# Kernel optimization log

Hardware: AMD Instinct MI355X
Metric: run time of the kernel (lower is better)

The kernel has to match this reference:

```python
import jax, jax.numpy as jnp
import numpy as np

G = 128        # grid resolution per axis (points are voxel centers on this grid)
N = 262144     # number of input points == number of output points
CIN = 16
COUT = 32


def _build_neighbors(inp_coords, out_coords):
    """Emulates FixedRadiusSearch(Linf, r=1.53*voxel) + invert_neighbors_list on a
    unit grid: for each output point and each of the 27 kernel taps t, find the
    (unique) input point at out_coord - (t-1), or -1 if that voxel is empty."""
    enc = lambda c: (c[:, 0].astype(np.int64) * G + c[:, 1]) * G + c[:, 2]
    inp_keys = enc(inp_coords)
    order = np.argsort(inp_keys)
    skeys = inp_keys[order]
    nbr = np.full((out_coords.shape[0], 27), -1, dtype=np.int32)
    k = 0
    for t0 in range(3):
        for t1 in range(3):
            for t2 in range(3):
                d = np.array([t0 - 1, t1 - 1, t2 - 1], dtype=np.int64)
                nc = out_coords - d  # input voxel s.t. (out - inp) == d
                valid = np.all((nc >= 0) & (nc < G), axis=1)
                keys = enc(np.clip(nc, 0, G - 1))
                pos = np.searchsorted(skeys, keys).clip(0, len(skeys) - 1)
                found = valid & (skeys[pos] == keys)
                nbr[:, k] = np.where(found, order[pos].astype(np.int32), -1)
                k += 1
    return nbr


def setup_inputs() -> dict:
    rng = np.random.default_rng(0)
    # unique voxels -> at most one point per voxel (regular-grid assumption)
    inp_keys = rng.choice(G ** 3, size=N, replace=False)
    out_keys = rng.choice(G ** 3, size=N, replace=False)
    dec = lambda kk: np.stack([kk // (G * G), (kk // G) % G, kk % G], axis=1).astype(np.int64)
    nbr_idx = jnp.asarray(_build_neighbors(dec(inp_keys), dec(out_keys)))

    key = jax.random.key(0)
    k1, k2 = jax.random.split(key)
    inp_features = jax.random.normal(k1, (N, CIN), dtype=jnp.float32)
    # matches kernel_initializer = uniform_(-0.05, 0.05)
    kernel = jax.random.uniform(k2, (3, 3, 3, CIN, COUT), dtype=jnp.float32,
                                minval=-0.05, maxval=0.05)
    bias = jnp.zeros((COUT,), dtype=jnp.float32)  # bias_initializer = zeros_
    return {"inp_features": inp_features, "kernel": kernel, "bias": bias,
            "nbr_idx": nbr_idx}


def reference(inp_features, kernel, bias, nbr_idx):
    # continuous_conv_transpose with interpolation='nearest_neighbor',
    # coordinate_mapping='identity', normalize=False on a unit grid:
    # out[j] = sum_t W[t] @ f[nbr(j, t)]  (missing taps contribute zero), + bias
    valid = (nbr_idx >= 0)
    idx = jnp.where(valid, nbr_idx, 0)
    gathered = inp_features[idx] * valid[..., None].astype(inp_features.dtype)  # [N,27,Cin]
    W = kernel.reshape(27, kernel.shape[-2], kernel.shape[-1])                  # [27,Cin,Cout]
    return jnp.einsum('nkc,kco->no', gathered, W) + bias
```

## Files before the change

### kernel.cpp

```cpp
#include <hip/hip_runtime.h>
#include <hip/hip_bf16.h>

#define NPTS  262144
#define CIN   16
#define COUT  32
#define NTAPS 27
#define BLK   512
#define DEPTH 12

typedef __attribute__((ext_vector_type(8)))  short short8v;
typedef __attribute__((ext_vector_type(16))) float f32x16;

__global__ __launch_bounds__(256) void cvt_feat_kernel(
    const float* __restrict__ feat, __hip_bfloat16* __restrict__ fb)
{
    const int i = blockIdx.x * 256 + threadIdx.x;
    const float4 x = ((const float4*)feat)[i];
    __hip_bfloat162* o = (__hip_bfloat162*)fb;
    o[2 * i]     = __float22bfloat162_rn(float2{x.x, x.y});
    o[2 * i + 1] = __float22bfloat162_rn(float2{x.z, x.w});
}

template<bool USE_WS>
__global__ __launch_bounds__(BLK, 3) void sct_mfma_kernel(
    const float* __restrict__ feat,
    const __hip_bfloat16* __restrict__ featb,
    const float* __restrict__ Wg,
    const float* __restrict__ bias,
    const int*   __restrict__ nbr,
    float*       __restrict__ out)
{
    __shared__ short bpack[NTAPS * 512];

    const int tid = threadIdx.x;
    for (int i = tid; i < NTAPS * 512; i += BLK) {
        const int tap  = i >> 9;
        const int r    = i & 511;
        const int ln   = r >> 3;
        const int e    = r & 7;
        const int cin  = ((ln >> 5) << 3) + e;
        const int cout = ln & 31;
        const __hip_bfloat16 h = __float2bfloat16(Wg[(tap * CIN + cin) * COUT + cout]);
        bpack[i] = *(const short*)&h;
    }
    __syncthreads();

    const int lane = tid & 63;
    const int wv   = tid >> 6;
    const int p0   = blockIdx.x * 256 + wv * 32;
    const int prow = lane & 31;
    const int g    = lane >> 5;
    const int* nb  = nbr + (long)(p0 + prow) * NTAPS;

    int nid[NTAPS];
    #pragma unroll
    for (int q = 0; q < 6; ++q) {
        const int4 v = *(const int4*)(nb + 4 * q);
        nid[4*q+0] = v.x; nid[4*q+1] = v.y; nid[4*q+2] = v.z; nid[4*q+3] = v.w;
    }
    {
        const int2 v2 = *(const int2*)(nb + 24);
        nid[24] = v2.x; nid[25] = v2.y; nid[26] = nb[26];
    }

    f32x16 acc;
    {
        const float b = bias[prow];
        #pragma unroll
        for (int r2 = 0; r2 < 16; ++r2) acc[r2] = b;
    }

    short8v af[DEPTH];

    auto gather1 = [&](int t, short8v& dst) {
        const int id = nid[t];
        short8v a = {};
        if (id >= 0) {
            if (USE_WS) {
                a = *(const short8v*)(featb + (long)id * CIN + g * 8);
            } else {
                const float4* fp = (const float4*)(feat + (long)id * CIN + g * 8);
                const float4 x = fp[0];
                const float4 y = fp[1];
                union { short8v v; __hip_bfloat162 h[4]; } u;
                u.h[0] = __float22bfloat162_rn(float2{x.x, x.y});
                u.h[1] = __float22bfloat162_rn(float2{x.z, x.w});
                u.h[2] = __float22bfloat162_rn(float2{y.x, y.y});
                u.h[3] = __float22bfloat162_rn(float2{y.z, y.w});
                a = u.v;
            }
        }
        dst = a;
    };

    #pragma unroll
    for (int t = 0; t < DEPTH; ++t) gather1(t, af[t]);

    #pragma unroll
    for (int t = 0; t < NTAPS; ++t) {
        const short8v bf = *(const short8v*)&bpack[(t << 9) + (lane << 3)];
        acc = __builtin_amdgcn_mfma_f32_32x32x16_bf16(af[t % DEPTH], bf, acc, 0, 0, 0);
        if (t + DEPTH < NTAPS) gather1(t + DEPTH, af[(t + DEPTH) % DEPTH]);
    }

    #pragma unroll
    for (int r2 = 0; r2 < 16; ++r2) {
        const int row = (r2 & 3) + 8 * (r2 >> 2) + 4 * g;
        out[(long)(p0 + row) * COUT + prow] = acc[r2];
    }
}

extern "C" void kernel_launch(void* const* d_in, const int* in_sizes, int n_in,
                              void* d_out, int out_size, void* d_ws, size_t ws_size,
                              hipStream_t stream) {
    const float* feat = (const float*)d_in[0];
    const float* Wg   = (const float*)d_in[1];
    const float* bias = (const float*)d_in[2];
    const int*   nbr  = (const int*)d_in[3];
    float*       out  = (float*)d_out;

    const size_t need = (size_t)NPTS * CIN * sizeof(__hip_bfloat16);
    if (ws_size >= need) {
        __hip_bfloat16* fb = (__hip_bfloat16*)d_ws;
        cvt_feat_kernel<<<NPTS * CIN / 4 / 256, 256, 0, stream>>>(feat, fb);
        sct_mfma_kernel<true><<<NPTS / 256, BLK, 0, stream>>>(feat, fb, Wg, bias, nbr, out);
    } else {
        sct_mfma_kernel<false><<<NPTS / 256, BLK, 0, stream>>>(feat, nullptr, Wg, bias, nbr, out);
    }
}
```

Baseline: 43.86 us.

## Precompute packed bf16 weight image in prep kernel and shrink blocks

The weight conversion and MFMA-layout packing moves out of every block into a one-off prep block, which writes a padded bf16 image to the workspace. Each conv block now fills LDS with a few vectorized 16-byte copies instead of strided scalar fp32 reads and converts. Blocks drop from 512 to 256 threads with a launch bound of 5, and gather depth falls from 12 to 8 to reduce register pressure. This is meant to raise occupancy and cut per-block setup, at the cost of twice as many blocks, each repeating the LDS fill.

```diff
diff --git a/kernel.cpp b/kernel.cpp
--- a/kernel.cpp
+++ b/kernel.cpp
@@ -5,49 +5,82 @@
 #define CIN   16
 #define COUT  32
 #define NTAPS 27
-#define BLK   512
-#define DEPTH 12
+#define BLK   256
+#define DEPTH 8
+
+#define WIMG_SHORTS (NTAPS * 512)
+#define WIMG_PAD    14336
+#define FEATB_OFF   32768
 
 typedef __attribute__((ext_vector_type(8)))  short short8v;
 typedef __attribute__((ext_vector_type(16))) float f32x16;
 
-__global__ __launch_bounds__(256) void cvt_feat_kernel(
-    const float* __restrict__ feat, __hip_bfloat16* __restrict__ fb)
+__global__ __launch_bounds__(256) void prep_kernel(
+    const float* __restrict__ feat, const float* __restrict__ Wg,
+    short* __restrict__ wimg, __hip_bfloat16* __restrict__ fb)
 {
-    const int i = blockIdx.x * 256 + threadIdx.x;
-    const float4 x = ((const float4*)feat)[i];
-    __hip_bfloat162* o = (__hip_bfloat162*)fb;
-    o[2 * i]     = __float22bfloat162_rn(float2{x.x, x.y});
-    o[2 * i + 1] = __float22bfloat162_rn(float2{x.z, x.w});
+    if (blockIdx.x < NPTS * CIN / 4 / 256) {
+        const int i = blockIdx.x * 256 + threadIdx.x;
+        const float4 x = ((const float4*)feat)[i];
+        __hip_bfloat162* o = (__hip_bfloat162*)fb;
+        o[2 * i]     = __float22bfloat162_rn(float2{x.x, x.y});
+        o[2 * i + 1] = __float22bfloat162_rn(float2{x.z, x.w});
+    } else {
+        for (int i = threadIdx.x; i < WIMG_PAD; i += 256) {
+            short v = 0;
+            if (i < WIMG_SHORTS) {
+                const int tap  = i >> 9;
+                const int r    = i & 511;
+                const int ln   = r >> 3;
+                const int e    = r & 7;
+                const int cin  = ((ln >> 5) << 3) + e;
+                const int cout = ln & 31;
+                const __hip_bfloat16 h =
+                    __float2bfloat16(Wg[(tap * CIN + cin) * COUT + cout]);
+                v = *(const short*)&h;
+            }
+            wimg[i] = v;
+        }
+    }
 }
 
 template<bool USE_WS>
-__global__ __launch_bounds__(BLK, 3) void sct_mfma_kernel(
+__global__ __launch_bounds__(BLK, 5) void sct_mfma_kernel(
     const float* __restrict__ feat,
     const __hip_bfloat16* __restrict__ featb,
+    const short* __restrict__ wimg,
     const float* __restrict__ Wg,
     const float* __restrict__ bias,
     const int*   __restrict__ nbr,
     float*       __restrict__ out)
 {
-    __shared__ short bpack[NTAPS * 512];
+    __shared__ short bpack[WIMG_PAD];
 
     const int tid = threadIdx.x;
-    for (int i = tid; i < NTAPS * 512; i += BLK) {
-        const int tap  = i >> 9;
-        const int r    = i & 511;
-        const int ln   = r >> 3;
-        const int e    = r & 7;
-        const int cin  = ((ln >> 5) << 3) + e;
-        const int cout = ln & 31;
-        const __hip_bfloat16 h = __float2bfloat16(Wg[(tap * CIN + cin) * COUT + cout]);
-        bpack[i] = *(const short*)&h;
+    if (USE_WS) {
+        #pragma unroll
+        for (int q = 0; q < 7; ++q) {
+            const int off = q * (256 * 8) + tid * 8;
+            *(short8v*)&bpack[off] = *(const short8v*)&wimg[off];
+        }
+    } else {
+        for (int i = tid; i < WIMG_SHORTS; i += BLK) {
+            const int tap  = i >> 9;
+            const int r    = i & 511;
+            const int ln   = r >> 3;
+            const int e    = r & 7;
+            const int cin  = ((ln >> 5) << 3) + e;
+            const int cout = ln & 31;
+            const __hip_bfloat16 h =
+                __float2bfloat16(Wg[(tap * CIN + cin) * COUT + cout]);
+            bpack[i] = *(const short*)&h;
+        }
     }
     __syncthreads();
 
     const int lane = tid & 63;
     const int wv   = tid >> 6;
-    const int p0   = blockIdx.x * 256 + wv * 32;
+    const int p0   = blockIdx.x * 128 + wv * 32;
     const int prow = lane & 31;
     const int g    = lane >> 5;
     const int* nb  = nbr + (long)(p0 + prow) * NTAPS;
@@ -119,12 +152,15 @@
     const int*   nbr  = (const int*)d_in[3];
     float*       out  = (float*)d_out;
 
-    const size_t need = (size_t)NPTS * CIN * sizeof(__hip_bfloat16);
+    const size_t need = FEATB_OFF + (size_t)NPTS * CIN * sizeof(__hip_bfloat16);
     if (ws_size >= need) {
-        __hip_bfloat16* fb = (__hip_bfloat16*)d_ws;
-        cvt_feat_kernel<<<NPTS * CIN / 4 / 256, 256, 0, stream>>>(feat, fb);
-        sct_mfma_kernel<true><<<NPTS / 256, BLK, 0, stream>>>(feat, fb, Wg, bias, nbr, out);
+        short* wimg = (short*)d_ws;
+        __hip_bfloat16* fb = (__hip_bfloat16*)((char*)d_ws + FEATB_OFF);
+        prep_kernel<<<NPTS * CIN / 4 / 256 + 1, 256, 0, stream>>>(feat, Wg, wimg, fb);
+        sct_mfma_kernel<true><<<NPTS / 128, BLK, 0, stream>>>(
+            feat, fb, wimg, Wg, bias, nbr, out);
     } else {
-        sct_mfma_kernel<false><<<NPTS / 256, BLK, 0, stream>>>(feat, nullptr, Wg, bias, nbr, out);
+        sct_mfma_kernel<false><<<NPTS / 128, BLK, 0, stream>>>(
+            feat, nullptr, nullptr, Wg, bias, nbr, out);
     }
 }
```

Result: slower. 49.58 us (+13.0%).
